# Kernel tuning notes

Measured on AMD Instinct MI355X. Metric: run time of the kernel, lower is better.

## Reference

```python
import jax, jax.numpy as jnp
import numpy as np

TEMP = 0.07


def setup_inputs() -> dict:
    key = jax.random.key(0)
    k1, k2 = jax.random.split(key)
    N, C = 8192, 512
    X = jax.random.normal(k1, (N, C), dtype=jnp.float32)
    Y = jax.random.normal(k2, (N, C), dtype=jnp.float32)
    return {"X": X, "Y": Y}


def reference(X, Y):
    # Original loop computes, per row i, cross-entropy over logits
    # [X_i.Y_i, X_i.Y_j (j != i)] / temp with label 0 (the positive).
    # Softmax CE is permutation-invariant, so this equals
    #   logsumexp(S_i / temp) - S_ii / temp,  S = X @ Y^T,
    # summed over rows (loop accumulates with +=, i.e. sum reduction).
    S = jnp.einsum('nc,mc->nm', X, Y) / TEMP  # [N, N]
    lse = jax.nn.logsumexp(S, axis=1)          # [N]
    pos = jnp.diagonal(S)                      # [N]
    return jnp.sum(lse - pos)
```

## Files before the change

### kernel.cpp

```cpp
#include <hip/hip_runtime.h>
#include <stdint.h>

#define N 8192
#define C 512
#define BM 128
#define BN 128
#define NSPLIT 8
#define COLS_PER_SPLIT (N / NSPLIT)
#define CT (COLS_PER_SPLIT / BN)
#define GRID_GEMM (64 * NSPLIT)
#define KSTEPS (C / 64)
#define INV_T 14.285714285714286f

typedef __attribute__((ext_vector_type(4)))  int   i32x4;
typedef __attribute__((ext_vector_type(8)))  int   i32x8;
typedef __attribute__((ext_vector_type(16))) float f32x16;

__global__ __launch_bounds__(256) void prep_kernel(const float* __restrict__ X,
                                                   const float* __restrict__ Y,
                                                   unsigned char* __restrict__ Xf8,
                                                   unsigned char* __restrict__ Yf8,
                                                   float* __restrict__ pos) {
  const int wave = threadIdx.x >> 6;
  const int lane = threadIdx.x & 63;
  const int row = blockIdx.x * 4 + wave;
  const float4* xr = (const float4*)(X + (size_t)row * C) + lane * 2;
  const float4* yr = (const float4*)(Y + (size_t)row * C) + lane * 2;
  float4 x0 = xr[0], x1 = xr[1];
  float4 y0 = yr[0], y1 = yr[1];
  float s = x0.x * y0.x + x0.y * y0.y + x0.z * y0.z + x0.w * y0.w
          + x1.x * y1.x + x1.y * y1.y + x1.z * y1.z + x1.w * y1.w;
  int2 ox, oy;
  ox.x = __builtin_amdgcn_cvt_pk_fp8_f32(x0.x, x0.y, 0, false);
  ox.x = __builtin_amdgcn_cvt_pk_fp8_f32(x0.z, x0.w, ox.x, true);
  ox.y = __builtin_amdgcn_cvt_pk_fp8_f32(x1.x, x1.y, 0, false);
  ox.y = __builtin_amdgcn_cvt_pk_fp8_f32(x1.z, x1.w, ox.y, true);
  oy.x = __builtin_amdgcn_cvt_pk_fp8_f32(y0.x, y0.y, 0, false);
  oy.x = __builtin_amdgcn_cvt_pk_fp8_f32(y0.z, y0.w, oy.x, true);
  oy.y = __builtin_amdgcn_cvt_pk_fp8_f32(y1.x, y1.y, 0, false);
  oy.y = __builtin_amdgcn_cvt_pk_fp8_f32(y1.z, y1.w, oy.y, true);
  ((int2*)(Xf8 + (size_t)row * C))[lane] = ox;
  ((int2*)(Yf8 + (size_t)row * C))[lane] = oy;
#pragma unroll
  for (int off = 32; off >= 1; off >>= 1) s += __shfl_xor(s, off);
  if (lane == 0) pos[row] = s * INV_T;
}

__global__ __launch_bounds__(256, 2) void gemm_lse_kernel(const unsigned char* __restrict__ Xf8,
                                                          const unsigned char* __restrict__ Yf8,
                                                          float2* __restrict__ partials) {
  __shared__ unsigned char Bs[BN][C];

  const int tid = threadIdx.x;
  const int bx = blockIdx.x;
  const int split = bx & (NSPLIT - 1);
  const int rb = bx >> 3;
  const int row0 = rb * BM;
  const int colbase = split * COLS_PER_SPLIT;

  const int w = tid >> 6;
  const int lane = tid & 63;
  const int lrow = lane & 31;
  const int h = lane >> 5;
  const int arow = w * 32 + lrow;
  const int swz = lrow & 7;

  i32x8 a_frag[KSTEPS];
#pragma unroll
  for (int s = 0; s < KSTEPS; ++s) {
    const unsigned char* ga = Xf8 + (size_t)(row0 + arow) * C + s * 64 + h * 32;
    i32x4 lo = *(const i32x4*)ga;
    i32x4 hi = *(const i32x4*)(ga + 16);
    a_frag[s] = i32x8{ lo[0], lo[1], lo[2], lo[3], hi[0], hi[1], hi[2], hi[3] };
  }

  float m_s[16], l_s[16];
#pragma unroll
  for (int s = 0; s < 16; ++s) { m_s[s] = -INFINITY; l_s[s] = 0.0f; }

  for (int ct = 0; ct < CT; ++ct) {
    const int col0 = colbase + ct * BN;
    f32x16 acc[4];
#pragma unroll
    for (int t = 0; t < 4; ++t)
#pragma unroll
      for (int e = 0; e < 16; ++e) acc[t][e] = 0.0f;

#pragma unroll
    for (int t = 0; t < 16; ++t) {
      const int s2 = t * 256 + tid;
      const int r = s2 >> 5;
      const int cir = s2 & 31;
      const int k0t = cir >> 3;
      const int p = cir & 7;
      const int jj = p ^ (r & 7);
      const unsigned char* gb = Yf8 + (size_t)(col0 + r) * C + k0t * 128 + jj * 16;
      uint32_t loff = (uint32_t)((t * 256 + (tid & ~63)) * 16);
      __builtin_amdgcn_global_load_lds(
          (const __attribute__((address_space(1))) uint32_t*)(uintptr_t)gb,
          (__attribute__((address_space(3))) uint32_t*)(uintptr_t)((char*)&Bs[0][0] + loff),
          16, 0, 0);
    }
    __syncthreads();

#pragma unroll
    for (int s = 0; s < KSTEPS; ++s) {
      const int seg = (s >> 1) * 128;
      const int c0 = (s & 1) * 4 + 2 * h;
#pragma unroll
      for (int tj = 0; tj < 4; ++tj) {
        const int brow = tj * 32 + lrow;
        i32x4 blo = *(const i32x4*)&Bs[brow][seg + (((c0    ) ^ swz) * 16)];
        i32x4 bhi = *(const i32x4*)&Bs[brow][seg + (((c0 + 1) ^ swz) * 16)];
        i32x8 bf = { blo[0], blo[1], blo[2], blo[3], bhi[0], bhi[1], bhi[2], bhi[3] };
        acc[tj] = __builtin_amdgcn_mfma_scale_f32_32x32x64_f8f6f4(
            a_frag[s], bf, acc[tj], 0, 0, 0, 127, 0, 127);
      }
    }

#pragma unroll
    for (int r = 0; r < 16; ++r) {
      float v0 = acc[0][r] * INV_T;
      float v1 = acc[1][r] * INV_T;
      float v2 = acc[2][r] * INV_T;
      float v3 = acc[3][r] * INV_T;
      float mx = fmaxf(fmaxf(v0, v1), fmaxf(v2, v3));
      float mn = fmaxf(m_s[r], mx);
      l_s[r] = l_s[r] * __expf(m_s[r] - mn)
             + __expf(v0 - mn) + __expf(v1 - mn) + __expf(v2 - mn) + __expf(v3 - mn);
      m_s[r] = mn;
    }
    __syncthreads();
  }

#pragma unroll
  for (int r = 0; r < 16; ++r) {
    float m = m_s[r], l = l_s[r];
#pragma unroll
    for (int off = 1; off < 32; off <<= 1) {
      float mo = __shfl_xor(m, off);
      float lo = __shfl_xor(l, off);
      float mn = fmaxf(m, mo);
      l = l * __expf(m - mn) + lo * __expf(mo - mn);
      m = mn;
    }
    m_s[r] = m; l_s[r] = l;
  }
  if (lrow == 0) {
#pragma unroll
    for (int r = 0; r < 16; ++r) {
      int row_local = (r & 3) + 8 * (r >> 2) + 4 * h;
      partials[(size_t)split * N + (row0 + w * 32 + row_local)] =
          make_float2(m_s[r], l_s[r]);
    }
  }
}

__global__ __launch_bounds__(256) void combine_kernel(const float2* __restrict__ partials,
                                                      const float* __restrict__ pos,
                                                      float* __restrict__ out) {
  int row = blockIdx.x * 256 + threadIdx.x;
  float M = -INFINITY, L = 0.0f;
#pragma unroll
  for (int s = 0; s < NSPLIT; ++s) {
    float2 pr = partials[(size_t)s * N + row];
    float mn = fmaxf(M, pr.x);
    L = L * __expf(M - mn) + pr.y * __expf(pr.x - mn);
    M = mn;
  }
  float v = M + __logf(L) - pos[row];
#pragma unroll
  for (int off = 32; off >= 1; off >>= 1) v += __shfl_xor(v, off);
  __shared__ float wsum[4];
  if ((threadIdx.x & 63) == 0) wsum[threadIdx.x >> 6] = v;
  __syncthreads();
  if (threadIdx.x == 0) atomicAdd(out, wsum[0] + wsum[1] + wsum[2] + wsum[3]);
}

extern "C" void kernel_launch(void* const* d_in, const int* in_sizes, int n_in,
                              void* d_out, int out_size, void* d_ws, size_t ws_size,
                              hipStream_t stream) {
  const float* X = (const float*)d_in[0];
  const float* Y = (const float*)d_in[1];
  float* out = (float*)d_out;

  char* w = (char*)d_ws;
  unsigned char* Xf8 = (unsigned char*)w;
  unsigned char* Yf8 = Xf8 + (size_t)N * C;
  float2* partials = (float2*)(Yf8 + (size_t)N * C);
  float* pos = (float*)((char*)partials + (size_t)NSPLIT * N * sizeof(float2));

  hipMemsetAsync(d_out, 0, sizeof(float), stream);
  prep_kernel<<<N / 4, 256, 0, stream>>>(X, Y, Xf8, Yf8, pos);
  gemm_lse_kernel<<<GRID_GEMM, 256, 0, stream>>>(Xf8, Yf8, partials);
  combine_kernel<<<N / 256, 256, 0, stream>>>(partials, pos, out);
}
```

Before: 126.7 us.

## Store B tile in MFMA fragment order in LDS and compute LSE in base 2

The B tile is now loaded into shared memory already arranged in MFMA operand order, so each lane reads contiguous 16-byte chunks at fixed offsets. This drops the XOR swizzle and the per-read address arithmetic. Logits are also prescaled by log2(e)/T so the online softmax can use exp2f and log2 directly, with a single ln2 multiply at the end. The risks are LDS bank conflicts from the new layout and small rounding differences from the base change.

```diff
diff --git a/kernel.cpp b/kernel.cpp
--- a/kernel.cpp
+++ b/kernel.cpp
@@ -10,7 +10,8 @@
 #define CT (COLS_PER_SPLIT / BN)
 #define GRID_GEMM (64 * NSPLIT)
 #define KSTEPS (C / 64)
-#define INV_T 14.285714285714286f
+#define U_SCALE 20.609929155556617f
+#define LN2 0.6931471805599453f
 
 typedef __attribute__((ext_vector_type(4)))  int   i32x4;
 typedef __attribute__((ext_vector_type(8)))  int   i32x8;
@@ -43,13 +44,13 @@
   ((int2*)(Yf8 + (size_t)row * C))[lane] = oy;
 #pragma unroll
   for (int off = 32; off >= 1; off >>= 1) s += __shfl_xor(s, off);
-  if (lane == 0) pos[row] = s * INV_T;
+  if (lane == 0) pos[row] = s * U_SCALE;
 }
 
 __global__ __launch_bounds__(256, 2) void gemm_lse_kernel(const unsigned char* __restrict__ Xf8,
                                                           const unsigned char* __restrict__ Yf8,
                                                           float2* __restrict__ partials) {
-  __shared__ unsigned char Bs[BN][C];
+  __shared__ unsigned char Bs[4096 * 16];
 
   const int tid = threadIdx.x;
   const int bx = blockIdx.x;
@@ -63,7 +64,6 @@
   const int lrow = lane & 31;
   const int h = lane >> 5;
   const int arow = w * 32 + lrow;
-  const int swz = lrow & 7;
 
   i32x8 a_frag[KSTEPS];
 #pragma unroll
@@ -78,6 +78,8 @@
 #pragma unroll
   for (int s = 0; s < 16; ++s) { m_s[s] = -INFINITY; l_s[s] = 0.0f; }
 
+  const unsigned char* bsr = &Bs[0] + lane * 16;
+
   for (int ct = 0; ct < CT; ++ct) {
     const int col0 = colbase + ct * BN;
     f32x16 acc[4];
@@ -88,30 +90,28 @@
 
 #pragma unroll
     for (int t = 0; t < 16; ++t) {
-      const int s2 = t * 256 + tid;
-      const int r = s2 >> 5;
-      const int cir = s2 & 31;
-      const int k0t = cir >> 3;
-      const int p = cir & 7;
-      const int jj = p ^ (r & 7);
-      const unsigned char* gb = Yf8 + (size_t)(col0 + r) * C + k0t * 128 + jj * 16;
+      const int L  = t * 256 + tid;
+      const int l6 = L & 63;
+      const int q  = (L >> 6) & 1;
+      const int tj = (L >> 7) & 3;
+      const int s  = L >> 9;
+      const unsigned char* gb = Yf8
+          + (size_t)(col0 + tj * 32 + (l6 & 31)) * C
+          + s * 64 + (l6 >> 5) * 32 + q * 16;
       uint32_t loff = (uint32_t)((t * 256 + (tid & ~63)) * 16);
       __builtin_amdgcn_global_load_lds(
           (const __attribute__((address_space(1))) uint32_t*)(uintptr_t)gb,
-          (__attribute__((address_space(3))) uint32_t*)(uintptr_t)((char*)&Bs[0][0] + loff),
+          (__attribute__((address_space(3))) uint32_t*)(uintptr_t)((char*)&Bs[0] + loff),
           16, 0, 0);
     }
     __syncthreads();
 
 #pragma unroll
     for (int s = 0; s < KSTEPS; ++s) {
-      const int seg = (s >> 1) * 128;
-      const int c0 = (s & 1) * 4 + 2 * h;
 #pragma unroll
       for (int tj = 0; tj < 4; ++tj) {
-        const int brow = tj * 32 + lrow;
-        i32x4 blo = *(const i32x4*)&Bs[brow][seg + (((c0    ) ^ swz) * 16)];
-        i32x4 bhi = *(const i32x4*)&Bs[brow][seg + (((c0 + 1) ^ swz) * 16)];
+        i32x4 blo = *(const i32x4*)(bsr + (s * 4 + tj) * 2048);
+        i32x4 bhi = *(const i32x4*)(bsr + (s * 4 + tj) * 2048 + 1024);
         i32x8 bf = { blo[0], blo[1], blo[2], blo[3], bhi[0], bhi[1], bhi[2], bhi[3] };
         acc[tj] = __builtin_amdgcn_mfma_scale_f32_32x32x64_f8f6f4(
             a_frag[s], bf, acc[tj], 0, 0, 0, 127, 0, 127);
@@ -120,14 +120,14 @@
 
 #pragma unroll
     for (int r = 0; r < 16; ++r) {
-      float v0 = acc[0][r] * INV_T;
-      float v1 = acc[1][r] * INV_T;
-      float v2 = acc[2][r] * INV_T;
-      float v3 = acc[3][r] * INV_T;
+      float v0 = acc[0][r] * U_SCALE;
+      float v1 = acc[1][r] * U_SCALE;
+      float v2 = acc[2][r] * U_SCALE;
+      float v3 = acc[3][r] * U_SCALE;
       float mx = fmaxf(fmaxf(v0, v1), fmaxf(v2, v3));
       float mn = fmaxf(m_s[r], mx);
-      l_s[r] = l_s[r] * __expf(m_s[r] - mn)
-             + __expf(v0 - mn) + __expf(v1 - mn) + __expf(v2 - mn) + __expf(v3 - mn);
+      l_s[r] = l_s[r] * exp2f(m_s[r] - mn)
+             + exp2f(v0 - mn) + exp2f(v1 - mn) + exp2f(v2 - mn) + exp2f(v3 - mn);
       m_s[r] = mn;
     }
     __syncthreads();
@@ -141,7 +141,7 @@
       float mo = __shfl_xor(m, off);
       float lo = __shfl_xor(l, off);
       float mn = fmaxf(m, mo);
-      l = l * __expf(m - mn) + lo * __expf(mo - mn);
+      l = l * exp2f(m - mn) + lo * exp2f(mo - mn);
       m = mn;
     }
     m_s[r] = m; l_s[r] = l;
@@ -165,16 +165,17 @@
   for (int s = 0; s < NSPLIT; ++s) {
     float2 pr = partials[(size_t)s * N + row];
     float mn = fmaxf(M, pr.x);
-    L = L * __expf(M - mn) + pr.y * __expf(pr.x - mn);
+    L = L * exp2f(M - mn) + pr.y * exp2f(pr.x - mn);
     M = mn;
   }
-  float v = M + __logf(L) - pos[row];
+  float v = M + __log2f(L) - pos[row];
 #pragma unroll
   for (int off = 32; off >= 1; off >>= 1) v += __shfl_xor(v, off);
   __shared__ float wsum[4];
   if ((threadIdx.x & 63) == 0) wsum[threadIdx.x >> 6] = v;
   __syncthreads();
-  if (threadIdx.x == 0) atomicAdd(out, wsum[0] + wsum[1] + wsum[2] + wsum[3]);
+  if (threadIdx.x == 0)
+    atomicAdd(out, LN2 * (wsum[0] + wsum[1] + wsum[2] + wsum[3]));
 }
 
 extern "C" void kernel_launch(void* const* d_in, const int* in_sizes, int n_in,
```

After: 138.0 us. 1.09x slower.

## Use 2x2 wave tiling with A reloaded from global, base-2 softmax math

Applied to the files above, without the earlier changes.

Reorganizes the four waves into a 2x2 grid, each computing a 64x64 sub-tile (two A row-halves times two B column-halves). This halves the LDS B-fragment reads per MFMA, at the cost of streaming A fragments from global/L2 per column tile in two K halves instead of keeping them all resident. The logsumexp now runs in base 2 (scale folds in log2 e, exp2f/log2f, final multiply by ln2), and the partials buffer doubles because each wave column emits its own partial row statistics.

```diff
diff --git a/kernel.cpp b/kernel.cpp
--- a/kernel.cpp
+++ b/kernel.cpp
@@ -9,8 +9,8 @@
 #define COLS_PER_SPLIT (N / NSPLIT)
 #define CT (COLS_PER_SPLIT / BN)
 #define GRID_GEMM (64 * NSPLIT)
-#define KSTEPS (C / 64)
-#define INV_T 14.285714285714286f
+#define U_SCALE 20.609929155556617f
+#define LN2 0.6931471805599453f
 
 typedef __attribute__((ext_vector_type(4)))  int   i32x4;
 typedef __attribute__((ext_vector_type(8)))  int   i32x8;
@@ -43,13 +43,13 @@
   ((int2*)(Yf8 + (size_t)row * C))[lane] = oy;
 #pragma unroll
   for (int off = 32; off >= 1; off >>= 1) s += __shfl_xor(s, off);
-  if (lane == 0) pos[row] = s * INV_T;
+  if (lane == 0) pos[row] = s * U_SCALE;
 }
 
 __global__ __launch_bounds__(256, 2) void gemm_lse_kernel(const unsigned char* __restrict__ Xf8,
                                                           const unsigned char* __restrict__ Yf8,
                                                           float2* __restrict__ partials) {
-  __shared__ unsigned char Bs[BN][C];
+  __shared__ unsigned char Bs[BN * 512];
 
   const int tid = threadIdx.x;
   const int bx = blockIdx.x;
@@ -62,29 +62,39 @@
   const int lane = tid & 63;
   const int lrow = lane & 31;
   const int h = lane >> 5;
-  const int arow = w * 32 + lrow;
+  const int wr = w >> 1;
+  const int wc = w & 1;
   const int swz = lrow & 7;
 
-  i32x8 a_frag[KSTEPS];
-#pragma unroll
-  for (int s = 0; s < KSTEPS; ++s) {
-    const unsigned char* ga = Xf8 + (size_t)(row0 + arow) * C + s * 64 + h * 32;
-    i32x4 lo = *(const i32x4*)ga;
-    i32x4 hi = *(const i32x4*)(ga + 16);
-    a_frag[s] = i32x8{ lo[0], lo[1], lo[2], lo[3], hi[0], hi[1], hi[2], hi[3] };
-  }
-
-  float m_s[16], l_s[16];
-#pragma unroll
-  for (int s = 0; s < 16; ++s) { m_s[s] = -INFINITY; l_s[s] = 0.0f; }
+  const unsigned char* Abase = Xf8 + (size_t)(row0 + wr * 64 + lrow) * C + h * 32;
+
+  i32x8 a[2][4];
+#define LOAD_A(kh)                                                         \
+  {                                                                        \
+    _Pragma("unroll")                                                      \
+    for (int sl = 0; sl < 4; ++sl)                                         \
+      _Pragma("unroll")                                                    \
+      for (int rh = 0; rh < 2; ++rh)                                       \
+        a[rh][sl] = *(const i32x8*)(Abase + (size_t)rh * 32 * C + ((kh)*4 + sl) * 64); \
+  }
+
+  LOAD_A(0)
+
+  float m_s[2][16], l_s[2][16];
+#pragma unroll
+  for (int rh = 0; rh < 2; ++rh)
+#pragma unroll
+    for (int r = 0; r < 16; ++r) { m_s[rh][r] = -INFINITY; l_s[rh][r] = 0.0f; }
 
   for (int ct = 0; ct < CT; ++ct) {
     const int col0 = colbase + ct * BN;
-    f32x16 acc[4];
-#pragma unroll
-    for (int t = 0; t < 4; ++t)
-#pragma unroll
-      for (int e = 0; e < 16; ++e) acc[t][e] = 0.0f;
+    f32x16 acc[2][2];
+#pragma unroll
+    for (int rh = 0; rh < 2; ++rh)
+#pragma unroll
+      for (int tj = 0; tj < 2; ++tj)
+#pragma unroll
+        for (int e = 0; e < 16; ++e) acc[rh][tj][e] = 0.0f;
 
 #pragma unroll
     for (int t = 0; t < 16; ++t) {
@@ -98,61 +108,75 @@
       uint32_t loff = (uint32_t)((t * 256 + (tid & ~63)) * 16);
       __builtin_amdgcn_global_load_lds(
           (const __attribute__((address_space(1))) uint32_t*)(uintptr_t)gb,
-          (__attribute__((address_space(3))) uint32_t*)(uintptr_t)((char*)&Bs[0][0] + loff),
+          (__attribute__((address_space(3))) uint32_t*)(uintptr_t)((char*)&Bs[0] + loff),
           16, 0, 0);
     }
     __syncthreads();
 
 #pragma unroll
-    for (int s = 0; s < KSTEPS; ++s) {
-      const int seg = (s >> 1) * 128;
-      const int c0 = (s & 1) * 4 + 2 * h;
-#pragma unroll
-      for (int tj = 0; tj < 4; ++tj) {
-        const int brow = tj * 32 + lrow;
-        i32x4 blo = *(const i32x4*)&Bs[brow][seg + (((c0    ) ^ swz) * 16)];
-        i32x4 bhi = *(const i32x4*)&Bs[brow][seg + (((c0 + 1) ^ swz) * 16)];
-        i32x8 bf = { blo[0], blo[1], blo[2], blo[3], bhi[0], bhi[1], bhi[2], bhi[3] };
-        acc[tj] = __builtin_amdgcn_mfma_scale_f32_32x32x64_f8f6f4(
-            a_frag[s], bf, acc[tj], 0, 0, 0, 127, 0, 127);
-      }
+    for (int kh = 0; kh < 2; ++kh) {
+#pragma unroll
+      for (int sl = 0; sl < 4; ++sl) {
+        const int s = kh * 4 + sl;
+        const int seg = (s >> 1) * 128;
+        const int c0 = (s & 1) * 4 + 2 * h;
+        i32x8 bf[2];
+#pragma unroll
+        for (int tj = 0; tj < 2; ++tj) {
+          const unsigned char* bp = &Bs[0] + (wc * 64 + tj * 32 + lrow) * 512 + seg;
+          i32x4 blo = *(const i32x4*)(bp + (((c0    ) ^ swz) * 16));
+          i32x4 bhi = *(const i32x4*)(bp + (((c0 + 1) ^ swz) * 16));
+          bf[tj] = i32x8{ blo[0], blo[1], blo[2], blo[3], bhi[0], bhi[1], bhi[2], bhi[3] };
+        }
+        acc[0][0] = __builtin_amdgcn_mfma_scale_f32_32x32x64_f8f6f4(a[0][sl], bf[0], acc[0][0], 0, 0, 0, 127, 0, 127);
+        acc[0][1] = __builtin_amdgcn_mfma_scale_f32_32x32x64_f8f6f4(a[0][sl], bf[1], acc[0][1], 0, 0, 0, 127, 0, 127);
+        acc[1][0] = __builtin_amdgcn_mfma_scale_f32_32x32x64_f8f6f4(a[1][sl], bf[0], acc[1][0], 0, 0, 0, 127, 0, 127);
+        acc[1][1] = __builtin_amdgcn_mfma_scale_f32_32x32x64_f8f6f4(a[1][sl], bf[1], acc[1][1], 0, 0, 0, 127, 0, 127);
+      }
+      if (kh == 0) LOAD_A(1)
     }
-
+    if (ct + 1 < CT) LOAD_A(0)
+
+#pragma unroll
+    for (int rh = 0; rh < 2; ++rh)
+#pragma unroll
+      for (int r = 0; r < 16; ++r) {
+        float v0 = acc[rh][0][r] * U_SCALE;
+        float v1 = acc[rh][1][r] * U_SCALE;
+        float mx = fmaxf(v0, v1);
+        float mn = fmaxf(m_s[rh][r], mx);
+        l_s[rh][r] = l_s[rh][r] * exp2f(m_s[rh][r] - mn)
+                   + exp2f(v0 - mn) + exp2f(v1 - mn);
+        m_s[rh][r] = mn;
+      }
+    __syncthreads();
+  }
+#undef LOAD_A
+
+#pragma unroll
+  for (int rh = 0; rh < 2; ++rh)
 #pragma unroll
     for (int r = 0; r < 16; ++r) {
-      float v0 = acc[0][r] * INV_T;
-      float v1 = acc[1][r] * INV_T;
-      float v2 = acc[2][r] * INV_T;
-      float v3 = acc[3][r] * INV_T;
-      float mx = fmaxf(fmaxf(v0, v1), fmaxf(v2, v3));
-      float mn = fmaxf(m_s[r], mx);
-      l_s[r] = l_s[r] * __expf(m_s[r] - mn)
-             + __expf(v0 - mn) + __expf(v1 - mn) + __expf(v2 - mn) + __expf(v3 - mn);
-      m_s[r] = mn;
+      float m = m_s[rh][r], l = l_s[rh][r];
+#pragma unroll
+      for (int off = 1; off < 32; off <<= 1) {
+        float mo = __shfl_xor(m, off);
+        float lo = __shfl_xor(l, off);
+        float mn = fmaxf(m, mo);
+        l = l * exp2f(m - mn) + lo * exp2f(mo - mn);
+        m = mn;
+      }
+      m_s[rh][r] = m; l_s[rh][r] = l;
     }
-    __syncthreads();
-  }
-
-#pragma unroll
-  for (int r = 0; r < 16; ++r) {
-    float m = m_s[r], l = l_s[r];
-#pragma unroll
-    for (int off = 1; off < 32; off <<= 1) {
-      float mo = __shfl_xor(m, off);
-      float lo = __shfl_xor(l, off);
-      float mn = fmaxf(m, mo);
-      l = l * __expf(m - mn) + lo * __expf(mo - mn);
-      m = mn;
-    }
-    m_s[r] = m; l_s[r] = l;
-  }
   if (lrow == 0) {
 #pragma unroll
-    for (int r = 0; r < 16; ++r) {
-      int row_local = (r & 3) + 8 * (r >> 2) + 4 * h;
-      partials[(size_t)split * N + (row0 + w * 32 + row_local)] =
-          make_float2(m_s[r], l_s[r]);
-    }
+    for (int rh = 0; rh < 2; ++rh)
+#pragma unroll
+      for (int r = 0; r < 16; ++r) {
+        int row_local = wr * 64 + rh * 32 + (r & 3) + 8 * (r >> 2) + 4 * h;
+        partials[(size_t)(split * 2 + wc) * N + (row0 + row_local)] =
+            make_float2(m_s[rh][r], l_s[rh][r]);
+      }
   }
 }
 
@@ -162,19 +186,20 @@
   int row = blockIdx.x * 256 + threadIdx.x;
   float M = -INFINITY, L = 0.0f;
 #pragma unroll
-  for (int s = 0; s < NSPLIT; ++s) {
+  for (int s = 0; s < 2 * NSPLIT; ++s) {
     float2 pr = partials[(size_t)s * N + row];
     float mn = fmaxf(M, pr.x);
-    L = L * __expf(M - mn) + pr.y * __expf(pr.x - mn);
+    L = L * exp2f(M - mn) + pr.y * exp2f(pr.x - mn);
     M = mn;
   }
-  float v = M + __logf(L) - pos[row];
+  float v = M + __log2f(L) - pos[row];
 #pragma unroll
   for (int off = 32; off >= 1; off >>= 1) v += __shfl_xor(v, off);
   __shared__ float wsum[4];
   if ((threadIdx.x & 63) == 0) wsum[threadIdx.x >> 6] = v;
   __syncthreads();
-  if (threadIdx.x == 0) atomicAdd(out, wsum[0] + wsum[1] + wsum[2] + wsum[3]);
+  if (threadIdx.x == 0)
+    atomicAdd(out, LN2 * (wsum[0] + wsum[1] + wsum[2] + wsum[3]));
 }
 
 extern "C" void kernel_launch(void* const* d_in, const int* in_sizes, int n_in,
@@ -188,7 +213,7 @@
   unsigned char* Xf8 = (unsigned char*)w;
   unsigned char* Yf8 = Xf8 + (size_t)N * C;
   float2* partials = (float2*)(Yf8 + (size_t)N * C);
-  float* pos = (float*)((char*)partials + (size_t)NSPLIT * N * sizeof(float2));
+  float* pos = (float*)((char*)partials + (size_t)2 * NSPLIT * N * sizeof(float2));
 
   hipMemsetAsync(d_out, 0, sizeof(float), stream);
   prep_kernel<<<N / 4, 256, 0, stream>>>(X, Y, Xf8, Yf8, pos);
```

Result: slower. 222.9 us (+75.9%).
